# Performance work log

Hardware: AMD Instinct MI355X
Metric: run time of the kernel (lower is better)

Reference implementation:

```python
import jax, jax.numpy as jnp
import numpy as np

NUM_SEQS = 4
SEQ_LEN = 1024  # 4 packed sequences of 1024 tokens -> S = 4096
NUM_HEADS = 16
HEAD_DIM = 64


def setup_inputs() -> dict:
    key = jax.random.key(0)
    k1, k2, k3 = jax.random.split(key, 3)
    S = NUM_SEQS * SEQ_LEN
    shape = (S, NUM_HEADS, HEAD_DIM)
    q = jax.random.normal(k1, shape, dtype=jnp.float32)
    k = jax.random.normal(k2, shape, dtype=jnp.float32)
    v = jax.random.normal(k3, shape, dtype=jnp.float32)
    # cumulative sequence lengths for the packed (flattened) batch
    cu_seqlens = (jnp.arange(NUM_SEQS + 1, dtype=jnp.int32) * SEQ_LEN)
    return {"q": q, "k": k, "v": v, "cu_seqlens": cu_seqlens, "bsz": 1}


def _block_diag_mask(s, cu_seqlens):
    # seq id of each packed position (bucketize against cu_seqlens[1:], right=True)
    positions = jnp.arange(s, dtype=jnp.int32)
    seq_ids = jnp.searchsorted(cu_seqlens[1:], positions, side='right')
    valid = positions < cu_seqlens[-1]
    same = (seq_ids[:, None] == seq_ids[None, :]) & (valid[:, None] & valid[None, :])
    return ~same  # True where attention is BLOCKED (cross-sequence)


def reference(q, k, v, cu_seqlens, bsz):
    # flattened-batch SDPA path with block-diagonal mask,
    # softmax_in_single_precision=True branch of VisionSdpaAttention
    s = q.shape[0] // bsz  # bsz == 1 (flatten_batch)
    scale = 1.0 / np.sqrt(q.shape[-1])
    blocked = _block_diag_mask(s, cu_seqlens)  # [s, s] bool

    # scores: [h, s, s]
    scores = jnp.einsum('shd,thd->hst', q, k) * scale
    add_mask = blocked.astype(q.dtype) * jnp.finfo(q.dtype).min
    scores = scores + add_mask[None, :, :]
    attn = jax.nn.softmax(scores.astype(jnp.float32), axis=-1).astype(q.dtype)
    # output: [s, h, d]
    out = jnp.einsum('hst,thd->shd', attn, v)
    return out
```

## Files before the change

### kernel.cpp

```cpp
#include <hip/hip_runtime.h>
#include <hip/hip_bf16.h>

#define NUM_HEADS 16
#define HEAD_DIM  64
#define HD        1024
#define SEQL      1024
#define NTILE     16
#define TILE_E    4096
#define HSTRIDE   (64 * TILE_E)
#define VT_OFF    (NUM_HEADS * HSTRIDE)
#define FIXED_M   12.0f
#define QK_SCALE  0.1803368801111204f

typedef __bf16 bf16x8 __attribute__((ext_vector_type(8)));
typedef float  f32x4  __attribute__((ext_vector_type(4)));

#define MFMA16(A, B, C) __builtin_amdgcn_mfma_f32_16x16x32_bf16((A), (B), (C), 0, 0, 0)
#define GLOAD_LDS16(gp, lp) \
  __builtin_amdgcn_global_load_lds((const __attribute__((address_space(1))) void*)(gp), \
                                   (__attribute__((address_space(3))) void*)(lp), 16, 0, 0)

__global__ __launch_bounds__(256)
void prep_kernel(const float* __restrict__ K, const float* __restrict__ V,
                 __bf16* __restrict__ ws)
{
    __shared__ __bf16 v_s[64][72];
    const int tid  = threadIdx.x;
    const int bx   = blockIdx.x;
    const int orig = (bx & 7) * 128 + (bx >> 3);
    const int h    = orig >> 6;
    const int tile = orig & 63;
    const int kv0  = tile * 64;
    __bf16* kb = ws + (size_t)h * HSTRIDE + (size_t)tile * TILE_E;
    __bf16* vt = ws + VT_OFF + (size_t)h * HSTRIDE + (size_t)tile * TILE_E;

    #pragma unroll
    for (int i = 0; i < 2; ++i) {
        const int c2 = tid + 256 * i;
        const int f  = c2 >> 6;
        const int l  = c2 & 63;
        const int g  = l >> 4, aa = l & 15;
        const int t  = f >> 1, cc = f & 1;
        const int r  = 16 * t + aa;
        const int d0 = 32 * cc + 8 * g;

        const float* kp = K + (size_t)(kv0 + r) * HD + h * HEAD_DIM + d0;
        float4 f0 = *(const float4*)kp, f1 = *(const float4*)(kp + 4);
        bf16x8 u = {(__bf16)(f0.x * QK_SCALE), (__bf16)(f0.y * QK_SCALE),
                    (__bf16)(f0.z * QK_SCALE), (__bf16)(f0.w * QK_SCALE),
                    (__bf16)(f1.x * QK_SCALE), (__bf16)(f1.y * QK_SCALE),
                    (__bf16)(f1.z * QK_SCALE), (__bf16)(f1.w * QK_SCALE)};
        *reinterpret_cast<bf16x8*>(kb + f * 512 + l * 8) = u;

        const float* vp = V + (size_t)(kv0 + r) * HD + h * HEAD_DIM + d0;
        float4 g0 = *(const float4*)vp, g1 = *(const float4*)(vp + 4);
        bf16x8 w = {(__bf16)g0.x, (__bf16)g0.y, (__bf16)g0.z, (__bf16)g0.w,
                    (__bf16)g1.x, (__bf16)g1.y, (__bf16)g1.z, (__bf16)g1.w};
        *reinterpret_cast<bf16x8*>(&v_s[r][d0]) = w;
    }
    __syncthreads();
    #pragma unroll
    for (int i = 0; i < 2; ++i) {
        const int c2 = tid + 256 * i;
        const int f  = c2 >> 6;
        const int l  = c2 & 63;
        const int g  = l >> 4, aa = l & 15;
        const int dt = f >> 1, cc = f & 1;
        const int d  = 16 * dt + aa;
        bf16x8 w;
        #pragma unroll
        for (int e = 0; e < 8; ++e) {
            const int kvl = 32 * cc + ((e >> 2) << 4) + 4 * g + (e & 3);
            w[e] = v_s[kvl][d];
        }
        *reinterpret_cast<bf16x8*>(vt + f * 512 + l * 8) = w;
    }
}

__global__ __launch_bounds__(512, 1)
void fattn19_kernel(const float* __restrict__ Q, const __bf16* __restrict__ ws,
                    float* __restrict__ O)
{
    extern __shared__ __bf16 lds[];

    const int tid  = threadIdx.x;
    const int lane = tid & 63;
    const int wave = tid >> 6;
    const int g    = lane >> 4;
    const int a    = lane & 15;

    const int b     = blockIdx.x;
    const int orig  = (b & 7) * 32 + (b >> 3);
    const int group = orig >> 2;
    const int qb    = orig & 3;
    const int h     = group >> 2;
    const int seq   = group & 3;
    const int q0    = seq * SEQL + qb * 256;

    const __bf16* kb_base = ws + (size_t)h * HSTRIDE + (size_t)seq * NTILE * TILE_E;
    const __bf16* vt_base = ws + VT_OFF + (size_t)h * HSTRIDE + (size_t)seq * NTILE * TILE_E;

    bf16x8 qf[2][2];
    #pragma unroll
    for (int u = 0; u < 2; ++u) {
        const float* qp = Q + (size_t)(q0 + wave * 32 + u * 16 + a) * HD + h * HEAD_DIM + g * 8;
        #pragma unroll
        for (int c = 0; c < 2; ++c) {
            float4 f0 = *reinterpret_cast<const float4*>(qp + 32 * c);
            float4 f1 = *reinterpret_cast<const float4*>(qp + 32 * c + 4);
            qf[u][c][0] = (__bf16)f0.x; qf[u][c][1] = (__bf16)f0.y;
            qf[u][c][2] = (__bf16)f0.z; qf[u][c][3] = (__bf16)f0.w;
            qf[u][c][4] = (__bf16)f1.x; qf[u][c][5] = (__bf16)f1.y;
            qf[u][c][6] = (__bf16)f1.z; qf[u][c][7] = (__bf16)f1.w;
        }
    }

    f32x4 o_acc[2][4];
    #pragma unroll
    for (int u = 0; u < 2; ++u)
        #pragma unroll
        for (int dt = 0; dt < 4; ++dt) o_acc[u][dt] = (f32x4){0.f, 0.f, 0.f, 0.f};
    f32x4 l_acc[2] = {(f32x4){0.f, 0.f, 0.f, 0.f}, (f32x4){0.f, 0.f, 0.f, 0.f}};

    bf16x8 ones;
    #pragma unroll
    for (int e = 0; e < 8; ++e) ones[e] = (__bf16)1.0f;

    const f32x4 minit = (f32x4){-FIXED_M, -FIXED_M, -FIXED_M, -FIXED_M};
    const int lb    = lane * 16;
    const int stid8 = tid * 8;

    auto stage_pair = [&](int p) {
        __bf16* base = lds + (size_t)(p & 3) * (4 * TILE_E);
        const __bf16* ks0 = kb_base + (size_t)(2 * p)     * TILE_E + stid8;
        const __bf16* ks1 = kb_base + (size_t)(2 * p + 1) * TILE_E + stid8;
        const __bf16* vs0 = vt_base + (size_t)(2 * p)     * TILE_E + stid8;
        const __bf16* vs1 = vt_base + (size_t)(2 * p + 1) * TILE_E + stid8;
        GLOAD_LDS16(ks0, base + stid8);
        GLOAD_LDS16(vs0, base + TILE_E + stid8);
        GLOAD_LDS16(ks1, base + 2 * TILE_E + stid8);
        GLOAD_LDS16(vs1, base + 3 * TILE_E + stid8);
    };

    auto pv = [&](const bf16x8 (&pfP)[2][2], const bf16x8 (&vfP)[8]) {
        __builtin_amdgcn_s_setprio(1);
        l_acc[0] = MFMA16(pfP[0][0], ones, l_acc[0]);
        l_acc[0] = MFMA16(pfP[0][1], ones, l_acc[0]);
        l_acc[1] = MFMA16(pfP[1][0], ones, l_acc[1]);
        l_acc[1] = MFMA16(pfP[1][1], ones, l_acc[1]);
        #pragma unroll
        for (int dt = 0; dt < 4; ++dt)
            #pragma unroll
            for (int u = 0; u < 2; ++u) {
                o_acc[u][dt] = MFMA16(pfP[u][0], vfP[2 * dt],     o_acc[u][dt]);
                o_acc[u][dt] = MFMA16(pfP[u][1], vfP[2 * dt + 1], o_acc[u][dt]);
            }
        __builtin_amdgcn_s_setprio(0);
    };

    bf16x8 pfA[2][2], pfB[2][2];
    bf16x8 vfA[8], vfB[8];

    auto body = [&](int t, bf16x8 (&pfC)[2][2], bf16x8 (&vfC)[8],
                    bf16x8 (&pfP)[2][2], bf16x8 (&vfP)[8]) {
        const char* kc = (const char*)lds +
                         (size_t)((t >> 1) & 3) * 32768 + (size_t)(t & 1) * 16384;
        const char* vc = kc + 8192;

        bf16x8 kf[8];
        #pragma unroll
        for (int f = 0; f < 8; ++f)
            kf[f] = *reinterpret_cast<const bf16x8*>(kc + f * 1024 + lb);

        if (t > 0) pv(pfP, vfP);

        f32x4 s[2][4];
        __builtin_amdgcn_s_setprio(1);
        #pragma unroll
        for (int q4 = 0; q4 < 4; ++q4) {
            s[0][q4] = MFMA16(kf[2 * q4],     qf[0][0], minit);
            s[0][q4] = MFMA16(kf[2 * q4 + 1], qf[0][1], s[0][q4]);
            s[1][q4] = MFMA16(kf[2 * q4],     qf[1][0], minit);
            s[1][q4] = MFMA16(kf[2 * q4 + 1], qf[1][1], s[1][q4]);
        }
        __builtin_amdgcn_s_setprio(0);

        #pragma unroll
        for (int f = 0; f < 8; ++f)
            vfC[f] = *reinterpret_cast<const bf16x8*>(vc + f * 1024 + lb);

        #pragma unroll
        for (int u = 0; u < 2; ++u)
            #pragma unroll
            for (int c = 0; c < 2; ++c)
                #pragma unroll
                for (int bb = 0; bb < 8; ++bb)
                    pfC[u][c][bb] = (__bf16)__builtin_amdgcn_exp2f(s[u][2 * c + (bb >> 2)][bb & 3]);
    };

    stage_pair(0);
    stage_pair(1);

    #pragma unroll
    for (int p = 0; p < 8; ++p) {
        if (p == 7) asm volatile("s_waitcnt vmcnt(0)" ::: "memory");
        else        asm volatile("s_waitcnt vmcnt(4)" ::: "memory");
        __builtin_amdgcn_sched_barrier(0);
        __builtin_amdgcn_s_barrier();
        __builtin_amdgcn_sched_barrier(0);
        if (p <= 5) stage_pair(p + 2);

        body(2 * p,     pfA, vfA, pfB, vfB);
        body(2 * p + 1, pfB, vfB, pfA, vfA);
    }
    pv(pfB, vfB);

    #pragma unroll
    for (int u = 0; u < 2; ++u)
        #pragma unroll
        for (int r = 0; r < 4; ++r) {
            const float inv = 1.0f / l_acc[u][r];
            float* op = O + (size_t)(q0 + wave * 32 + u * 16 + 4 * g + r) * HD + h * HEAD_DIM + a;
            #pragma unroll
            for (int dt = 0; dt < 4; ++dt)
                op[16 * dt] = o_acc[u][dt][r] * inv;
        }
}

extern "C" void kernel_launch(void* const* d_in, const int* in_sizes, int n_in,
                              void* d_out, int out_size, void* d_ws, size_t ws_size,
                              hipStream_t stream) {
    const float* q = (const float*)d_in[0];
    const float* k = (const float*)d_in[1];
    const float* v = (const float*)d_in[2];
    float* out = (float*)d_out;
    __bf16* ws = (__bf16*)d_ws;

    hipFuncSetAttribute((const void*)fattn19_kernel,
                        hipFuncAttributeMaxDynamicSharedMemorySize, 4 * 4 * TILE_E * 2);

    prep_kernel<<<1024, 256, 0, stream>>>(k, v, ws);
    fattn19_kernel<<<256, 512, 4 * 4 * TILE_E * 2, stream>>>(q, ws, out);
}
```

Baseline: 33.60 us.

## Preload all V tiles into LDS and stream only K through a ring

The attention kernel now copies all 16 V^T tiles for its sequence and head into LDS at kernel start. Only K tiles stream through a 4-slot ring buffer, two tiles per iteration. The wait in each iteration becomes a full vmcnt(0) drain. This is meant to simplify the staging and cut per-iteration load traffic, but it puts all V loads ahead of the first compute step, raises LDS use to 160KB, and drops the partial-wait overlap.

Measured after the change: 34.39 us. 2.4% more time.

```diff
diff --git a/kernel.cpp b/kernel.cpp
--- a/kernel.cpp
+++ b/kernel.cpp
@@ -78,7 +78,7 @@
 }
 
 __global__ __launch_bounds__(512, 1)
-void fattn19_kernel(const float* __restrict__ Q, const __bf16* __restrict__ ws,
+void fattn21_kernel(const float* __restrict__ Q, const __bf16* __restrict__ ws,
                     float* __restrict__ O)
 {
     extern __shared__ __bf16 lds[];
@@ -100,6 +100,8 @@
     const __bf16* kb_base = ws + (size_t)h * HSTRIDE + (size_t)seq * NTILE * TILE_E;
     const __bf16* vt_base = ws + VT_OFF + (size_t)h * HSTRIDE + (size_t)seq * NTILE * TILE_E;
 
+    __bf16* kbuf = lds + NTILE * TILE_E;
+
     bf16x8 qf[2][2];
     #pragma unroll
     for (int u = 0; u < 2; ++u) {
@@ -130,16 +132,9 @@
     const int lb    = lane * 16;
     const int stid8 = tid * 8;
 
-    auto stage_pair = [&](int p) {
-        __bf16* base = lds + (size_t)(p & 3) * (4 * TILE_E);
-        const __bf16* ks0 = kb_base + (size_t)(2 * p)     * TILE_E + stid8;
-        const __bf16* ks1 = kb_base + (size_t)(2 * p + 1) * TILE_E + stid8;
-        const __bf16* vs0 = vt_base + (size_t)(2 * p)     * TILE_E + stid8;
-        const __bf16* vs1 = vt_base + (size_t)(2 * p + 1) * TILE_E + stid8;
-        GLOAD_LDS16(ks0, base + stid8);
-        GLOAD_LDS16(vs0, base + TILE_E + stid8);
-        GLOAD_LDS16(ks1, base + 2 * TILE_E + stid8);
-        GLOAD_LDS16(vs1, base + 3 * TILE_E + stid8);
+    auto stage_k = [&](int t) {
+        GLOAD_LDS16(kb_base + (size_t)t * TILE_E + stid8,
+                    kbuf + (size_t)(t & 3) * TILE_E + stid8);
     };
 
     auto pv = [&](const bf16x8 (&pfP)[2][2], const bf16x8 (&vfP)[8]) {
@@ -163,9 +158,8 @@
 
     auto body = [&](int t, bf16x8 (&pfC)[2][2], bf16x8 (&vfC)[8],
                     bf16x8 (&pfP)[2][2], bf16x8 (&vfP)[8]) {
-        const char* kc = (const char*)lds +
-                         (size_t)((t >> 1) & 3) * 32768 + (size_t)(t & 1) * 16384;
-        const char* vc = kc + 8192;
+        const char* kc = (const char*)kbuf + (size_t)(t & 3) * 8192;
+        const char* vc = (const char*)lds + (size_t)t * 8192;
 
         bf16x8 kf[8];
         #pragma unroll
@@ -198,17 +192,18 @@
                     pfC[u][c][bb] = (__bf16)__builtin_amdgcn_exp2f(s[u][2 * c + (bb >> 2)][bb & 3]);
     };
 
-    stage_pair(0);
-    stage_pair(1);
+    #pragma unroll
+    for (int t = 0; t < NTILE; ++t)
+        GLOAD_LDS16(vt_base + (size_t)t * TILE_E + stid8, lds + (size_t)t * TILE_E + stid8);
+    stage_k(0); stage_k(1);
 
     #pragma unroll
     for (int p = 0; p < 8; ++p) {
-        if (p == 7) asm volatile("s_waitcnt vmcnt(0)" ::: "memory");
-        else        asm volatile("s_waitcnt vmcnt(4)" ::: "memory");
+        asm volatile("s_waitcnt vmcnt(0)" ::: "memory");
         __builtin_amdgcn_sched_barrier(0);
         __builtin_amdgcn_s_barrier();
         __builtin_amdgcn_sched_barrier(0);
-        if (p <= 5) stage_pair(p + 2);
+        if (p <= 6) { stage_k(2 * p + 2); stage_k(2 * p + 3); }
 
         body(2 * p,     pfA, vfA, pfB, vfB);
         body(2 * p + 1, pfB, vfB, pfA, vfA);
@@ -236,9 +231,10 @@
     float* out = (float*)d_out;
     __bf16* ws = (__bf16*)d_ws;
 
-    hipFuncSetAttribute((const void*)fattn19_kernel,
-                        hipFuncAttributeMaxDynamicSharedMemorySize, 4 * 4 * TILE_E * 2);
+    const int lds_bytes = (NTILE + 4) * TILE_E * 2;
+    hipFuncSetAttribute((const void*)fattn21_kernel,
+                        hipFuncAttributeMaxDynamicSharedMemorySize, lds_bytes);
 
     prep_kernel<<<1024, 256, 0, stream>>>(k, v, ws);
-    fattn19_kernel<<<256, 512, 4 * 4 * TILE_E * 2, stream>>>(q, ws, out);
+    fattn21_kernel<<<256, 512, lds_bytes, stream>>>(q, ws, out);
 }
```
